# Kernel optimization log

Measured on AMD Instinct MI355X. Metric: run time of the kernel, lower is better.

## Reference

```python
import jax, jax.numpy as jnp
import numpy as np

N = 100000   # nodes
E = 1600000  # edges
D_IN = 128
D_H = 128


def setup_inputs() -> dict:
    key = jax.random.key(0)
    ks = jax.random.split(key, 8)
    s = 1.0 / np.sqrt(D_IN)
    return {
        "x": jax.random.normal(ks[0], (N, D_IN), dtype=jnp.float32),
        "edge_index": jax.random.randint(ks[1], (2, E), 0, N, dtype=jnp.int64),
        "W_l1": jax.random.uniform(ks[2], (D_IN, D_H), jnp.float32, -s, s),
        "b_l1": jnp.zeros((D_H,), jnp.float32),
        "W_r1": jax.random.uniform(ks[3], (D_IN, D_H), jnp.float32, -s, s),
        "W_l2": jax.random.uniform(ks[4], (D_H, D_H), jnp.float32, -s, s),
        "b_l2": jnp.zeros((D_H,), jnp.float32),
        "W_r2": jax.random.uniform(ks[5], (D_H, D_H), jnp.float32, -s, s),
    }


def _sage_layer(z, src, dst, Wl, bl, Wr):
    # message: relu(x_j) gathered along src; aggregate: mean over dst
    msg = jax.nn.relu(z[src])                                   # [E, D]
    summed = jax.ops.segment_sum(msg, dst, num_segments=N)      # [N, D]
    cnt = jax.ops.segment_sum(jnp.ones((src.shape[0],), z.dtype), dst,
                              num_segments=N)                   # [N]
    mean = summed / jnp.maximum(cnt, 1.0)[:, None]
    return mean @ Wl + bl + z @ Wr                              # lin_l + lin_r(root)


def reference(x, edge_index, W_l1, b_l1, W_r1, W_l2, b_l2, W_r2):
    src, dst = edge_index[0], edge_index[1]
    h = _sage_layer(x, src, dst, W_l1, b_l1, W_r1)
    h = jax.nn.relu(h)  # activation between layers; norms are Identity, dropout 0
    return _sage_layer(h, src, dst, W_l2, b_l2, W_r2)
```

## Files before the change

kernel.cpp:

```cpp
#include <hip/hip_runtime.h>

typedef short short8 __attribute__((ext_vector_type(8)));
typedef unsigned short ushort8 __attribute__((ext_vector_type(8)));
typedef float f32x4 __attribute__((ext_vector_type(4)));
typedef float f32x2 __attribute__((ext_vector_type(2)));

__device__ __forceinline__ unsigned short f2bf(float f) {
    unsigned int u = __float_as_uint(f);
    u += 0x7FFFu + ((u >> 16) & 1u);
    return (unsigned short)(u >> 16);
}
__device__ __forceinline__ float bf2f(unsigned short s) {
    return __uint_as_float(((unsigned int)s) << 16);
}


#define BSHIFT 8
#define BCAP   8192
#define EPB    2048

__global__ __launch_bounds__(256) void p1_k(const int* __restrict__ ei,
                                            int* __restrict__ bcnt,
                                            unsigned int* __restrict__ bbuf,
                                            int E, int B) {
    __shared__ int s_cnt[512];
    __shared__ int s_base[512];
    int tid = threadIdx.x;
    for (int b = tid; b < B; b += 256) s_cnt[b] = 0;
    __syncthreads();

    int e0 = blockIdx.x * EPB + tid;
    int dstc[8];
#pragma unroll
    for (int k = 0; k < 8; k++) {
        int e = e0 + k * 256;
        dstc[k] = (e < E) ? ei[E + e] : -1;
        if (e < E) atomicAdd(&s_cnt[dstc[k] >> BSHIFT], 1);
    }
    __syncthreads();
    for (int b = tid; b < B; b += 256) {
        int c = s_cnt[b];
        s_base[b] = c ? atomicAdd(&bcnt[b], c) : 0;
        s_cnt[b] = 0;
    }
    __syncthreads();
#pragma unroll
    for (int k = 0; k < 8; k++) {
        int e = e0 + k * 256;
        if (e < E) {
            int src = ei[e];
            int dst = dstc[k];
            int b = dst >> BSHIFT;
            int pos = s_base[b] + atomicAdd(&s_cnt[b], 1);
            if (pos < BCAP)
                bbuf[(size_t)b * BCAP + pos] = ((unsigned int)(dst & 255) << 17) | (unsigned int)src;
        }
    }
}

__global__ __launch_bounds__(256) void p2_k(const unsigned int* __restrict__ bbuf,
                                            const int* __restrict__ bcnt,
                                            int* __restrict__ col,
                                            int* __restrict__ deg, int N) {
    __shared__ int s_deg[256];
    int tid = threadIdx.x;
    int b = blockIdx.x;
    s_deg[tid] = 0;
    __syncthreads();
    int cnt = bcnt[b];
    if (cnt > BCAP) cnt = BCAP;
    int nbase = b << BSHIFT;
    for (int i = tid; i < cnt; i += 256) {
        unsigned int p = bbuf[(size_t)b * BCAP + i];
        int src = (int)(p & 0x1FFFFu);
        int rem = (int)(p >> 17);
        int slot = atomicAdd(&s_deg[rem], 1);
        if (slot < 64) col[(size_t)(nbase + rem) * 64 + slot] = src;
    }
    __syncthreads();
    int n = nbase + tid;
    if (n < N) {
        int d = s_deg[tid];
        deg[n] = d;
        int dc = min(d, 64);
        int pe = min((dc + 3) & ~3, 64);
        for (int j = dc; j < pe; j++) col[(size_t)n * 64 + j] = N;
    }
}


__global__ void cvt_x_k(const float* __restrict__ x, unsigned short* __restrict__ xb,
                        unsigned int* __restrict__ xq, unsigned int* __restrict__ hqz,
                        int total4) {
    int i = blockIdx.x * 256 + threadIdx.x;
    if (i < total4) {
        float4 v = ((const float4*)x)[i];
        ushort4 p;
        p.x = f2bf(v.x); p.y = f2bf(v.y); p.z = f2bf(v.z); p.w = f2bf(v.w);
        ((ushort4*)xb)[i] = p;
        float rx = fmaxf(v.x, 0.f), ry = fmaxf(v.y, 0.f);
        float rz = fmaxf(v.z, 0.f), rw = fmaxf(v.w, 0.f);
        unsigned int q = (unsigned int)__builtin_amdgcn_cvt_pk_fp8_f32(rx, ry, 0, false);
        q = (unsigned int)__builtin_amdgcn_cvt_pk_fp8_f32(rz, rw, (int)q, true);
        xq[i] = q;
    } else if (i < total4 + 32) {
        ushort4 z; z.x = 0; z.y = 0; z.z = 0; z.w = 0;
        ((ushort4*)xb)[i] = z;
        xq[i] = 0;
        hqz[i - total4] = 0;
    }
}

__global__ void cvt_w_k(const float* __restrict__ W0, const float* __restrict__ W1,
                        const float* __restrict__ W2, const float* __restrict__ W3,
                        unsigned short* __restrict__ wsz) {
    int idx = blockIdx.x * 256 + threadIdx.x;
    if (idx >= 4 * 16384) return;
    int m = idx >> 14, r = idx & 16383;
    const float* W = (m == 0) ? W0 : (m == 1) ? W1 : (m == 2) ? W2 : W3;
    int k = r >> 7, n = r & 127;
    int t = k >> 5, kg = (k >> 3) & 3, j = k & 7;
    int c = n >> 4, ln = n & 15;
    int dst = (((t * 8 + c) * 64) + kg * 16 + ln) * 8 + j;
    wsz[m * 16384 + dst] = f2bf(W[r]);
}


__global__ __launch_bounds__(256) void agg_q(const unsigned char* __restrict__ hq,
                                             const int* __restrict__ col,
                                             const int* __restrict__ deg,
                                             unsigned short* __restrict__ mean,
                                             int N) {
    int lane = threadIdx.x & 63;
    int g = lane >> 4, l16 = lane & 15;
    int n = (blockIdx.x * 4 + (threadIdx.x >> 6)) * 4 + g;
    if (n >= N) return;
    int m = deg[n];
    if (m > 64) m = 64;
    const int* cp = col + (size_t)n * 64;
    unsigned int lofs = (unsigned int)l16 * 8u;

    f32x2 a[4];
#pragma unroll
    for (int d = 0; d < 4; d++) { a[d].x = 0.f; a[d].y = 0.f; }

    int s0 = cp[0], s1 = cp[1], s2 = cp[2], s3 = cp[3];

#pragma unroll 2
    for (int i = 0; i < m; i += 4) {
        uint2 v0 = *(const uint2*)(hq + ((((unsigned int)s0) << 7) + lofs));
        uint2 v1 = *(const uint2*)(hq + ((((unsigned int)s1) << 7) + lofs));
        uint2 v2 = *(const uint2*)(hq + ((((unsigned int)s2) << 7) + lofs));
        uint2 v3 = *(const uint2*)(hq + ((((unsigned int)s3) << 7) + lofs));
        s0 = cp[i + 4]; s1 = cp[i + 5]; s2 = cp[i + 6]; s3 = cp[i + 7];
#pragma unroll
        for (int k = 0; k < 4; k++) {
            uint2 v = (k == 0) ? v0 : (k == 1) ? v1 : (k == 2) ? v2 : v3;
            f32x2 p0 = __builtin_amdgcn_cvt_pk_f32_fp8((int)v.x, false);
            f32x2 p1 = __builtin_amdgcn_cvt_pk_f32_fp8((int)v.x, true);
            f32x2 p2 = __builtin_amdgcn_cvt_pk_f32_fp8((int)v.y, false);
            f32x2 p3 = __builtin_amdgcn_cvt_pk_f32_fp8((int)v.y, true);
            asm("v_pk_add_f32 %0, %0, %1" : "+v"(a[0]) : "v"(p0));
            asm("v_pk_add_f32 %0, %0, %1" : "+v"(a[1]) : "v"(p1));
            asm("v_pk_add_f32 %0, %0, %1" : "+v"(a[2]) : "v"(p2));
            asm("v_pk_add_f32 %0, %0, %1" : "+v"(a[3]) : "v"(p3));
        }
    }

    float iv = 1.0f / (float)max(m, 1);
    ushort8 p;
#pragma unroll
    for (int d = 0; d < 4; d++) {
        p[2 * d]     = f2bf(a[d].x * iv);
        p[2 * d + 1] = f2bf(a[d].y * iv);
    }
    *(ushort8*)((char*)mean + ((((unsigned int)n) << 8) + (unsigned int)l16 * 16u)) = p;
}


template <bool RELU, bool OUT_BF16, bool OUT_Q>
__global__ __launch_bounds__(256) void gemm_fused(const unsigned short* __restrict__ A,
                                                  const unsigned short* __restrict__ Z,
                                                  const unsigned short* __restrict__ wsz,
                                                  const float* __restrict__ bias,
                                                  float* __restrict__ outF,
                                                  unsigned short* __restrict__ outB,
                                                  unsigned char* __restrict__ outQ,
                                                  int M, int NG) {
    __shared__ unsigned short smem[32768];
    {
        const int4* src = (const int4*)wsz;
        int4* dst = (int4*)smem;
        for (int i = threadIdx.x; i < 4096; i += 256) dst[i] = src[i];
    }
    __syncthreads();

    int lane = threadIdx.x & 63;
    int wv = threadIdx.x >> 6;
    int r16 = lane & 15, kg = lane >> 4;

    for (int gq = blockIdx.x * 4 + wv; gq < NG; gq += gridDim.x * 4) {
        int rbase = gq * 64;
        short8 af[4][4], zf[4][4];
#pragma unroll
        for (int i = 0; i < 4; i++) {
            int row = rbase + i * 16 + r16;
            if (row < M) {
                const short8* ap = (const short8*)(A + (size_t)row * 128);
                const short8* zp = (const short8*)(Z + (size_t)row * 128);
#pragma unroll
                for (int t = 0; t < 4; t++) {
                    af[i][t] = ap[t * 4 + kg];
                    zf[i][t] = zp[t * 4 + kg];
                }
            } else {
                short8 zr = {0, 0, 0, 0, 0, 0, 0, 0};
#pragma unroll
                for (int t = 0; t < 4; t++) { af[i][t] = zr; zf[i][t] = zr; }
            }
        }
#pragma unroll
        for (int c = 0; c < 8; c++) {
            float bv = bias[c * 16 + r16];
            f32x4 acc[4];
#pragma unroll
            for (int i = 0; i < 4; i++) acc[i] = (f32x4){bv, bv, bv, bv};
#pragma unroll
            for (int t = 0; t < 4; t++) {
                short8 wa = *(const short8*)(smem + ((t * 8 + c) * 64 + lane) * 8);
#pragma unroll
                for (int i = 0; i < 4; i++)
                    acc[i] = __builtin_amdgcn_mfma_f32_16x16x32_bf16(af[i][t], wa, acc[i], 0, 0, 0);
            }
#pragma unroll
            for (int t = 0; t < 4; t++) {
                short8 wb = *(const short8*)(smem + 16384 + ((t * 8 + c) * 64 + lane) * 8);
#pragma unroll
                for (int i = 0; i < 4; i++)
                    acc[i] = __builtin_amdgcn_mfma_f32_16x16x32_bf16(zf[i][t], wb, acc[i], 0, 0, 0);
            }
#pragma unroll
            for (int i = 0; i < 4; i++) {
#pragma unroll
                for (int r = 0; r < 4; r++) {
                    int orow = rbase + i * 16 + kg * 4 + r;
                    if (orow < M) {
                        float v = acc[i][r];
                        if (RELU) v = fmaxf(v, 0.f);
                        if (OUT_BF16)
                            outB[(size_t)orow * 128 + c * 16 + r16] = f2bf(v);
                        else
                            outF[(size_t)orow * 128 + c * 16 + r16] = v;
                        if (OUT_Q) {
                            unsigned int q = (unsigned int)__builtin_amdgcn_cvt_pk_fp8_f32(v, v, 0, false);
                            outQ[(size_t)orow * 128 + c * 16 + r16] = (unsigned char)(q & 0xFFu);
                        }
                    }
                }
            }
        }
    }
}


extern "C" void kernel_launch(void* const* d_in, const int* in_sizes, int n_in,
                              void* d_out, int out_size, void* d_ws, size_t ws_size,
                              hipStream_t stream) {
    const float* x   = (const float*)d_in[0];
    const int*   ei  = (const int*)d_in[1];
    const float* Wl1 = (const float*)d_in[2];
    const float* bl1 = (const float*)d_in[3];
    const float* Wr1 = (const float*)d_in[4];
    const float* Wl2 = (const float*)d_in[5];
    const float* bl2 = (const float*)d_in[6];
    const float* Wr2 = (const float*)d_in[7];

    int N = in_sizes[0] / 128;
    int E = in_sizes[1] / 2;
    int B = (N + 255) >> BSHIFT;

    char* ws = (char*)d_ws;
    size_t off = 0;
    auto alloc = [&](size_t bytes) -> char* {
        char* p = ws + off;
        off += (bytes + 255) & ~(size_t)255;
        return p;
    };
    int*   deg  = (int*)alloc((size_t)N * 4);
    int*   bcnt = (int*)alloc((size_t)B * 4);
    unsigned short* xb    = (unsigned short*)alloc((size_t)(N + 1) * 128 * 2);
    unsigned short* meanB = (unsigned short*)alloc((size_t)N * 128 * 2);
    unsigned short* hb    = (unsigned short*)alloc((size_t)(N + 1) * 128 * 2);
    unsigned short* wsz   = (unsigned short*)alloc(4 * 16384 * 2);

    unsigned int* bbuf = (unsigned int*)meanB;
    unsigned int* xq   = (unsigned int*)hb;
    int* col = (int*)d_out;
    unsigned char* hq = (unsigned char*)d_out + (size_t)N * 64 * 4;

    hipMemsetAsync(bcnt, 0, (size_t)B * 4, stream);

    p1_k<<<(E + EPB - 1) / EPB, 256, 0, stream>>>(ei, bcnt, bbuf, E, B);
    p2_k<<<B, 256, 0, stream>>>(bbuf, bcnt, col, deg, N);

    int total4 = N * 32;
    cvt_x_k<<<(total4 + 32 + 255) / 256, 256, 0, stream>>>(
        x, xb, xq, (unsigned int*)(hq + (size_t)N * 128), total4);
    cvt_w_k<<<(4 * 16384 + 255) / 256, 256, 0, stream>>>(Wl1, Wr1, Wl2, Wr2, wsz);

    int NT = (N + 15) / 16;
    int NG = (NT + 3) / 4;
    int GB = (NG + 3) / 4;
    agg_q<<<(N + 15) / 16, 256, 0, stream>>>((const unsigned char*)xq, col, deg, meanB, N);
    gemm_fused<true, true, true><<<GB, 256, 0, stream>>>(meanB, xb, wsz, bl1,
                                                         nullptr, hb, hq, N, NG);
    agg_q<<<(N + 15) / 16, 256, 0, stream>>>(hq, col, deg, meanB, N);
    gemm_fused<false, false, false><<<GB, 256, 0, stream>>>(meanB, hb, wsz + 32768, bl2,
                                                            (float*)d_out, nullptr, nullptr, N, NG);
}
```

Measured before the change: 291.9 us.

## Stage bucketed edges in LDS and write padded 8-word groups coalesced

The edge bucketing kernel now uses 512 threads and gives each bucket a segment padded to a multiple of 8. It prefix-sums the padded counts and scatters each entry into a shared-memory staging array. The staged entries are then copied to global memory in 32-byte groups, which is meant to replace scattered single-word global writes with contiguous ones. Padding slots are filled with a sentinel that the second pass skips, at the cost of more shared memory, extra barriers for the scan, and more bucket capacity used by padding.

```diff
diff --git a/kernel.cpp b/kernel.cpp
--- a/kernel.cpp
+++ b/kernel.cpp
@@ -18,43 +18,72 @@
 #define BSHIFT 8
 #define BCAP   8192
 #define EPB    2048
-
-__global__ __launch_bounds__(256) void p1_k(const int* __restrict__ ei,
+#define STG    4792
+
+__global__ __launch_bounds__(512) void p1_k(const int* __restrict__ ei,
                                             int* __restrict__ bcnt,
                                             unsigned int* __restrict__ bbuf,
                                             int E, int B) {
     __shared__ int s_cnt[512];
-    __shared__ int s_base[512];
+    __shared__ int s_cur[512];
+    __shared__ int s_off[512];
+    __shared__ unsigned int s_gmap[608];
+    __shared__ unsigned int stage[STG];
+    __shared__ int s_T;
     int tid = threadIdx.x;
-    for (int b = tid; b < B; b += 256) s_cnt[b] = 0;
+    s_cnt[tid] = 0;
+    for (int i = tid; i < STG; i += 512) stage[i] = 0xFFFFFFFFu;
     __syncthreads();
 
     int e0 = blockIdx.x * EPB + tid;
-    int dstc[8];
-#pragma unroll
-    for (int k = 0; k < 8; k++) {
-        int e = e0 + k * 256;
+    int dstc[4];
+#pragma unroll
+    for (int k = 0; k < 4; k++) {
+        int e = e0 + k * 512;
         dstc[k] = (e < E) ? ei[E + e] : -1;
         if (e < E) atomicAdd(&s_cnt[dstc[k] >> BSHIFT], 1);
     }
     __syncthreads();
-    for (int b = tid; b < B; b += 256) {
-        int c = s_cnt[b];
-        s_base[b] = c ? atomicAdd(&bcnt[b], c) : 0;
-        s_cnt[b] = 0;
-    }
-    __syncthreads();
-#pragma unroll
-    for (int k = 0; k < 8; k++) {
-        int e = e0 + k * 256;
+    int c = s_cnt[tid];
+    int cpad = (c + 7) & ~7;
+    s_off[tid] = cpad;
+    __syncthreads();
+    for (int d = 1; d < 512; d <<= 1) {
+        int v = s_off[tid];
+        int add = (tid >= d) ? s_off[tid - d] : 0;
+        __syncthreads();
+        s_off[tid] = v + add;
+        __syncthreads();
+    }
+    if (tid == 511) s_T = s_off[511];
+    __syncthreads();
+    int excl = s_off[tid] - cpad;
+    int gbase = (c > 0) ? atomicAdd(&bcnt[tid], cpad) : 0;
+    int ng = cpad >> 3;
+    unsigned int bb = (unsigned int)tid * BCAP;
+    for (int k = 0; k < ng; k++) {
+        int gw = gbase + (k << 3);
+        s_gmap[(excl >> 3) + k] = (gw + 8 <= BCAP) ? (bb + (unsigned int)gw) : 0xFFFFFFFFu;
+    }
+    s_off[tid] = excl;
+    s_cur[tid] = 0;
+    __syncthreads();
+#pragma unroll
+    for (int k = 0; k < 4; k++) {
+        int e = e0 + k * 512;
         if (e < E) {
             int src = ei[e];
             int dst = dstc[k];
             int b = dst >> BSHIFT;
-            int pos = s_base[b] + atomicAdd(&s_cnt[b], 1);
-            if (pos < BCAP)
-                bbuf[(size_t)b * BCAP + pos] = ((unsigned int)(dst & 255) << 17) | (unsigned int)src;
+            int pos = s_off[b] + atomicAdd(&s_cur[b], 1);
+            stage[pos] = ((unsigned int)(dst & 255) << 17) | (unsigned int)src;
         }
+    }
+    __syncthreads();
+    int T = s_T;
+    for (int i = tid; i < T; i += 512) {
+        unsigned int g = s_gmap[i >> 3];
+        if (g != 0xFFFFFFFFu) bbuf[(size_t)g + (i & 7)] = stage[i];
     }
 }
 
@@ -72,6 +101,7 @@
     int nbase = b << BSHIFT;
     for (int i = tid; i < cnt; i += 256) {
         unsigned int p = bbuf[(size_t)b * BCAP + i];
+        if (p == 0xFFFFFFFFu) continue;
         int src = (int)(p & 0x1FFFFu);
         int rem = (int)(p >> 17);
         int slot = atomicAdd(&s_deg[rem], 1);
@@ -300,7 +330,7 @@
 
     hipMemsetAsync(bcnt, 0, (size_t)B * 4, stream);
 
-    p1_k<<<(E + EPB - 1) / EPB, 256, 0, stream>>>(ei, bcnt, bbuf, E, B);
+    p1_k<<<(E + EPB - 1) / EPB, 512, 0, stream>>>(ei, bcnt, bbuf, E, B);
     p2_k<<<B, 256, 0, stream>>>(bbuf, bcnt, col, deg, N);
 
     int total4 = N * 32;
```

After: 281.7 us. 3.5% less time.
